# Kernel tuning notes

Hardware: AMD Instinct MI355X
Metric: run time of the kernel (lower is better)

The kernel has to match this reference:

```python
import jax, jax.numpy as jnp
import numpy as np

B, L, D, H = 8, 1024, 1024, 16
K = D // H

def setup_inputs() -> dict:
    key = jax.random.key(0)
    k1, k2, k3 = jax.random.split(key, 3)
    scale = 1.0 / np.sqrt(D)
    return {
        "x": jax.random.normal(k1, (B, L, D), dtype=jnp.float32),
        "w_in": jax.random.normal(k2, (D, 3 * D), dtype=jnp.float32) * scale,
        "b_in": jnp.zeros((3 * D,), dtype=jnp.float32),
        "w_out": jax.random.normal(k3, (D, D), dtype=jnp.float32) * scale,
        "b_out": jnp.zeros((D,), dtype=jnp.float32),
    }

def reference(x, w_in, b_in, w_out, b_out):
    # Fused QKV projection: [B, L, 3D]
    qkv = x @ w_in + b_in
    q, k, v = jnp.split(qkv, 3, axis=-1)
    # [B, L, D] -> [B, H, L, K]
    def to_heads(t):
        return t.reshape(B, L, H, K).transpose(0, 2, 1, 3)
    q, k, v = to_heads(q), to_heads(k), to_heads(v)
    # Full [B, H, L, L] score matrix (non-flash, as in source)
    logits = jnp.einsum('bhlk,bhmk->bhlm', q, k) / jnp.sqrt(jnp.float32(K))
    # NOTE: the source computes softmax but then (bug, reproduced faithfully)
    # uses the raw logits in the value contraction. causal_mask defaults False.
    out = jnp.einsum('bhlm,bhmk->bhlk', logits, v)
    out = out.transpose(0, 2, 1, 3).reshape(B, L, D)
    return out @ w_out + b_out
```

## Files before the change

### kernel.cpp

```cpp
#include <hip/hip_runtime.h>
#include <hip/hip_bf16.h>


typedef __attribute__((ext_vector_type(8))) short short8;
typedef __attribute__((ext_vector_type(4))) float f32x4;

static __device__ __forceinline__ short f2bf(float f) {
  __hip_bfloat16 h = __float2bfloat16(f);
  return __builtin_bit_cast(short, h);
}
static __device__ __forceinline__ float bf2f(short s) {
  unsigned int u = ((unsigned int)(unsigned short)s) << 16;
  return __builtin_bit_cast(float, u);
}

#define GLOAD16(src, dst)                                        \
  __builtin_amdgcn_global_load_lds(                              \
      (const __attribute__((address_space(1))) void*)(src),      \
      (__attribute__((address_space(3))) void*)(dst), 16, 0, 0)

static __device__ __forceinline__ void transpose_body(
    const float* __restrict__ in, __hip_bfloat16* __restrict__ out,
    int R, int C, int c0, int r0, float tile[32][33]) {
  int tx = threadIdx.x & 31;
  int ty = threadIdx.x >> 5;
#pragma unroll
  for (int i = 0; i < 4; ++i)
    tile[ty + i * 8][tx] = in[(size_t)(r0 + ty + i * 8) * C + c0 + tx];
  __syncthreads();
#pragma unroll
  for (int i = 0; i < 4; ++i)
    out[(size_t)(c0 + ty + i * 8) * R + r0 + tx] =
        __float2bfloat16(tile[tx][ty + i * 8]);
}

__global__ __launch_bounds__(256) void prep_kernel(
    const float* __restrict__ x, __hip_bfloat16* __restrict__ x_bf,
    const float* __restrict__ w_in, __hip_bfloat16* __restrict__ w_inT,
    const float* __restrict__ w_out, __hip_bfloat16* __restrict__ w_outT) {
  __shared__ float tile[32][33];
  const int bx = blockIdx.x;
  if (bx < 4096) {
    size_t i = ((size_t)bx * 256 + threadIdx.x) * 8;
    float4 v0 = *(const float4*)(x + i);
    float4 v1 = *(const float4*)(x + i + 4);
    short8 o;
    o[0] = f2bf(v0.x); o[1] = f2bf(v0.y); o[2] = f2bf(v0.z); o[3] = f2bf(v0.w);
    o[4] = f2bf(v1.x); o[5] = f2bf(v1.y); o[6] = f2bf(v1.z); o[7] = f2bf(v1.w);
    *(short8*)((__hip_bfloat16*)x_bf + i) = o;
  } else if (bx < 4096 + 3072) {
    int b = bx - 4096;
    transpose_body(w_in, w_inT, 1024, 3072, (b % 96) * 32, (b / 96) * 32, tile);
  } else {
    int b = bx - 7168;
    transpose_body(w_out, w_outT, 1024, 1024, (b % 32) * 32, (b / 32) * 32, tile);
  }
}

static __device__ __forceinline__ void store_out(__hip_bfloat16* p, float v) {
  *p = __float2bfloat16(v);
}
static __device__ __forceinline__ void store_out(float* p, float v) { *p = v; }

template <typename OutT, int KD, int AS, int NBN, int NOUT, long BTB>
__global__ __launch_bounds__(256) void gemm_bt_kernel(
    const __hip_bfloat16* __restrict__ A, const __hip_bfloat16* __restrict__ Bt,
    const float* __restrict__ bias, OutT* __restrict__ C) {
  __shared__ __align__(16) __hip_bfloat16 As[2][128 * 32];
  __shared__ __align__(16) __hip_bfloat16 Bs[2][128 * 32];

  const int t = threadIdx.x;
  A += (size_t)blockIdx.y * 1024 * AS;
  Bt += (size_t)blockIdx.y * BTB;
  C += (size_t)blockIdx.y * 1024 * NOUT;

  const int cpx = gridDim.x >> 3;
  const int wg = (blockIdx.x & 7) * cpx + (blockIdx.x >> 3);
  const int bm = wg / NBN, bn = wg % NBN;
  const int m0 = bm * 128, n0 = bn * 128;

  const int w = t >> 6, lane = t & 63;
  const int wr = w >> 1, wc = w & 1;
  const int lr = lane & 15, kg = lane >> 4;

  const int g0 = w * 128 + lane;
  const int g1 = g0 + 64;
  const __hip_bfloat16* srcA0 = A + (size_t)(m0 + (g0 >> 2)) * AS + (g0 & 3) * 8;
  const __hip_bfloat16* srcA1 = A + (size_t)(m0 + (g1 >> 2)) * AS + (g1 & 3) * 8;
  const __hip_bfloat16* srcB0 = Bt + (size_t)(n0 + (g0 >> 2)) * KD + (g0 & 3) * 8;
  const __hip_bfloat16* srcB1 = Bt + (size_t)(n0 + (g1 >> 2)) * KD + (g1 & 3) * 8;
  const int lds0 = w * 128 * 8;
  const int lds1 = (w * 128 + 64) * 8;

  f32x4 acc[4][4] = {};
  constexpr int steps = KD / 32;

  GLOAD16(srcA0, &As[0][lds0]);
  GLOAD16(srcA1, &As[0][lds1]);
  GLOAD16(srcB0, &Bs[0][lds0]);
  GLOAD16(srcB1, &Bs[0][lds1]);
  __syncthreads();

  int cur = 0;
#pragma unroll 1
  for (int kt = 0; kt < steps; ++kt) {
    if (kt + 1 < steps) {
      const int ko = (kt + 1) * 32;
      GLOAD16(srcA0 + ko, &As[cur ^ 1][lds0]);
      GLOAD16(srcA1 + ko, &As[cur ^ 1][lds1]);
      GLOAD16(srcB0 + ko, &Bs[cur ^ 1][lds0]);
      GLOAD16(srcB1 + ko, &Bs[cur ^ 1][lds1]);
    }
    const __hip_bfloat16* Ac = As[cur];
    const __hip_bfloat16* Bc = Bs[cur];
    short8 af[4], bfv[4];
#pragma unroll
    for (int mi = 0; mi < 4; ++mi)
      af[mi] = *(const short8*)&Ac[(wr * 64 + mi * 16 + lr) * 32 + kg * 8];
#pragma unroll
    for (int ni = 0; ni < 4; ++ni)
      bfv[ni] = *(const short8*)&Bc[(wc * 64 + ni * 16 + lr) * 32 + kg * 8];
#pragma unroll
    for (int mi = 0; mi < 4; ++mi)
#pragma unroll
      for (int ni = 0; ni < 4; ++ni)
        acc[mi][ni] = __builtin_amdgcn_mfma_f32_16x16x32_bf16(
            af[mi], bfv[ni], acc[mi][ni], 0, 0, 0);
    __syncthreads();
    cur ^= 1;
  }

#pragma unroll
  for (int mi = 0; mi < 4; ++mi) {
    int row0 = m0 + wr * 64 + mi * 16 + kg * 4;
#pragma unroll
    for (int ni = 0; ni < 4; ++ni) {
      int col = n0 + wc * 64 + ni * 16 + lr;
      float bv = bias[col];
#pragma unroll
      for (int r = 0; r < 4; ++r)
        store_out(&C[(size_t)(row0 + r) * NOUT + col], acc[mi][ni][r] + bv);
    }
  }
}

__global__ __launch_bounds__(256) void ktv_kernel(
    const __hip_bfloat16* __restrict__ qkv, float* __restrict__ Spart) {
  __shared__ __align__(16) float Ks[64][68];
  __shared__ __align__(16) float Vs[64][68];
  const int bh = blockIdx.x;
  const int ch = blockIdx.y;
  const int b = bh >> 4, h = bh & 15;
  const __hip_bfloat16* base = qkv + (size_t)b * 1024 * 3072;
  const int hoff = h * 64;
  const int t = threadIdx.x;
  const int i0 = (t >> 4) * 4;
  const int j0 = (t & 15) * 4;
  const int srow = t >> 2;
  const int sg0 = t & 3;

  f32x4 acc[4] = {};

  for (int c = 0; c < 2; ++c) {
    int l0 = ch * 128 + c * 64;
#pragma unroll
    for (int rep = 0; rep < 2; ++rep) {
      int g = sg0 + rep * 4;
      const __hip_bfloat16* rowp = base + (size_t)(l0 + srow) * 3072;
      short8 kv = *(const short8*)(rowp + 1024 + hoff + g * 8);
      short8 vv = *(const short8*)(rowp + 2048 + hoff + g * 8);
      f32x4 k0, k1, v0, v1;
#pragma unroll
      for (int e = 0; e < 4; ++e) {
        k0[e] = bf2f(kv[e]); k1[e] = bf2f(kv[4 + e]);
        v0[e] = bf2f(vv[e]); v1[e] = bf2f(vv[4 + e]);
      }
      *(f32x4*)&Ks[srow][g * 8] = k0;
      *(f32x4*)&Ks[srow][g * 8 + 4] = k1;
      *(f32x4*)&Vs[srow][g * 8] = v0;
      *(f32x4*)&Vs[srow][g * 8 + 4] = v1;
    }
    __syncthreads();
#pragma unroll 8
    for (int l = 0; l < 64; ++l) {
      f32x4 kq = *(const f32x4*)&Ks[l][i0];
      f32x4 vq = *(const f32x4*)&Vs[l][j0];
#pragma unroll
      for (int ii = 0; ii < 4; ++ii) acc[ii] += kq[ii] * vq;
    }
    __syncthreads();
  }

  float* Sp = Spart + ((size_t)ch * 128 + bh) * 4096;
#pragma unroll
  for (int ii = 0; ii < 4; ++ii)
#pragma unroll
    for (int jj = 0; jj < 4; ++jj)
      Sp[(i0 + ii) * 64 + j0 + jj] = acc[ii][jj];
}

__global__ __launch_bounds__(512) void ut_kernel(
    const float* __restrict__ Spart, const __hip_bfloat16* __restrict__ w_outT,
    __hip_bfloat16* __restrict__ Ut) {
  __shared__ __align__(16) __hip_bfloat16 Sl[64][72];
  const int bh = blockIdx.x;
  const int b = bh >> 4, h = bh & 15;
  const int t = threadIdx.x, w = t >> 6, lane = t & 63;
  const int lr = lane & 15, kg = lane >> 4;

#pragma unroll
  for (int rep = 0; rep < 2; ++rep) {
    int e4 = t + rep * 512;
    int row = e4 >> 4, c4 = e4 & 15;
    f32x4 s = {};
#pragma unroll
    for (int c = 0; c < 8; ++c)
      s += *(const f32x4*)&Spart[((size_t)c * 128 + bh) * 4096 + row * 64 + c4 * 4];
    s *= 0.125f;
    __hip_bfloat16* p = &Sl[row][c4 * 4];
    p[0] = __float2bfloat16(s[0]); p[1] = __float2bfloat16(s[1]);
    p[2] = __float2bfloat16(s[2]); p[3] = __float2bfloat16(s[3]);
  }
  __syncthreads();

  const __hip_bfloat16* Ap = w_outT + (size_t)(w * 128 + lr) * 1024 + h * 64 + kg * 8;
  short8 bF[4][2];
#pragma unroll
  for (int ni = 0; ni < 4; ++ni)
#pragma unroll
    for (int kk = 0; kk < 2; ++kk)
      bF[ni][kk] = *(const short8*)&Sl[ni * 16 + lr][kk * 32 + kg * 8];

  f32x4 acc[8][4] = {};
#pragma unroll
  for (int mi = 0; mi < 8; ++mi) {
#pragma unroll
    for (int kk = 0; kk < 2; ++kk) {
      short8 aF = *(const short8*)(Ap + (size_t)mi * 16 * 1024 + kk * 32);
#pragma unroll
      for (int ni = 0; ni < 4; ++ni)
        acc[mi][ni] = __builtin_amdgcn_mfma_f32_16x16x32_bf16(
            aF, bF[ni][kk], acc[mi][ni], 0, 0, 0);
    }
  }

  __hip_bfloat16* Up = Ut + (size_t)b * 1024 * 1024;
#pragma unroll
  for (int mi = 0; mi < 8; ++mi) {
    int row0 = w * 128 + mi * 16 + kg * 4;
#pragma unroll
    for (int ni = 0; ni < 4; ++ni) {
      int col = h * 64 + ni * 16 + lr;
#pragma unroll
      for (int r = 0; r < 4; ++r)
        Up[(size_t)(row0 + r) * 1024 + col] = __float2bfloat16(acc[mi][ni][r]);
    }
  }
}

extern "C" void kernel_launch(void* const* d_in, const int* in_sizes, int n_in,
                              void* d_out, int out_size, void* d_ws, size_t ws_size,
                              hipStream_t stream) {
  const float* x = (const float*)d_in[0];
  const float* w_in = (const float*)d_in[1];
  const float* b_in = (const float*)d_in[2];
  const float* w_out = (const float*)d_in[3];
  const float* b_out = (const float*)d_in[4];
  float* out = (float*)d_out;

  char* ws = (char*)d_ws;
  __hip_bfloat16* x_bf = (__hip_bfloat16*)ws;   ws += (size_t)8192 * 1024 * 2;
  __hip_bfloat16* w_inT = (__hip_bfloat16*)ws;  ws += (size_t)3072 * 1024 * 2;
  __hip_bfloat16* w_outT = (__hip_bfloat16*)ws; ws += (size_t)1024 * 1024 * 2;
  __hip_bfloat16* qkv = (__hip_bfloat16*)ws;    ws += (size_t)8192 * 3072 * 2;
  float* Spart = (float*)ws;                    ws += (size_t)8 * 128 * 64 * 64 * 4;
  __hip_bfloat16* Ut = (__hip_bfloat16*)ws;     ws += (size_t)8 * 1024 * 1024 * 2;

  prep_kernel<<<8192, 256, 0, stream>>>(x, x_bf, w_in, w_inT, w_out, w_outT);

  gemm_bt_kernel<__hip_bfloat16, 1024, 1024, 24, 3072, 0>
      <<<dim3(1536, 1), 256, 0, stream>>>(x_bf, w_inT, b_in, qkv);

  ktv_kernel<<<dim3(128, 8), 256, 0, stream>>>(qkv, Spart);

  ut_kernel<<<128, 512, 0, stream>>>(Spart, w_outT, Ut);

  gemm_bt_kernel<float, 1024, 3072, 8, 1024, 1024 * 1024>
      <<<dim3(64, 8), 256, 0, stream>>>(qkv, Ut, b_out, out);
}
```

Baseline: 142.4 us.

## Triple-buffer GEMM LDS with vmcnt waits, XOR swizzle, and tile remap

Moves the bf16 GEMM mainloop from double to triple buffering. Loads are issued two k-steps ahead and each step waits with explicit s_waitcnt vmcnt plus raw barriers, so global-to-LDS traffic overlaps more MFMA work. It also XOR-swizzles the LDS layout to reduce bank conflicts on the short8 fragment reads. For the QKV GEMM (NBN==24) it remaps blocks so each XCD works on a grouped set of tiles for better L2 reuse. The cost is 50% more shared memory per block, which may lower occupancy, and hand-written wait counts that must match the number of loads in flight.

```diff
diff --git a/kernel.cpp b/kernel.cpp
--- a/kernel.cpp
+++ b/kernel.cpp
@@ -18,6 +18,10 @@
   __builtin_amdgcn_global_load_lds(                              \
       (const __attribute__((address_space(1))) void*)(src),      \
       (__attribute__((address_space(3))) void*)(dst), 16, 0, 0)
+#define BAR() __builtin_amdgcn_s_barrier()
+#define SCHED() __builtin_amdgcn_sched_barrier(0)
+#define WAIT_VM4() asm volatile("s_waitcnt vmcnt(4)" ::: "memory")
+#define WAIT_VM0() asm volatile("s_waitcnt vmcnt(0)" ::: "memory")
 
 static __device__ __forceinline__ void transpose_body(
     const float* __restrict__ in, __hip_bfloat16* __restrict__ out,
@@ -66,17 +70,27 @@
 __global__ __launch_bounds__(256) void gemm_bt_kernel(
     const __hip_bfloat16* __restrict__ A, const __hip_bfloat16* __restrict__ Bt,
     const float* __restrict__ bias, OutT* __restrict__ C) {
-  __shared__ __align__(16) __hip_bfloat16 As[2][128 * 32];
-  __shared__ __align__(16) __hip_bfloat16 Bs[2][128 * 32];
+  __shared__ __align__(16) __hip_bfloat16 As[3][128 * 32];
+  __shared__ __align__(16) __hip_bfloat16 Bs[3][128 * 32];
 
   const int t = threadIdx.x;
   A += (size_t)blockIdx.y * 1024 * AS;
   Bt += (size_t)blockIdx.y * BTB;
   C += (size_t)blockIdx.y * 1024 * NOUT;
 
-  const int cpx = gridDim.x >> 3;
-  const int wg = (blockIdx.x & 7) * cpx + (blockIdx.x >> 3);
-  const int bm = wg / NBN, bn = wg % NBN;
+  const int xcd = blockIdx.x & 7;
+  const int c = blockIdx.x >> 3;
+  int bm, bn;
+  if constexpr (NBN == 24) {
+    const int st = c >> 4;
+    const int im = (c >> 2) & 3, in_ = c & 3;
+    bm = xcd * 8 + (st & 1) * 4 + im;
+    bn = (st >> 1) * 4 + in_;
+  } else {
+    const int cpx = gridDim.x >> 3;
+    const int wg = xcd * cpx + c;
+    bm = wg / NBN; bn = wg % NBN;
+  }
   const int m0 = bm * 128, n0 = bn * 128;
 
   const int w = t >> 6, lane = t & 63;
@@ -85,49 +99,68 @@
 
   const int g0 = w * 128 + lane;
   const int g1 = g0 + 64;
-  const __hip_bfloat16* srcA0 = A + (size_t)(m0 + (g0 >> 2)) * AS + (g0 & 3) * 8;
-  const __hip_bfloat16* srcA1 = A + (size_t)(m0 + (g1 >> 2)) * AS + (g1 & 3) * 8;
-  const __hip_bfloat16* srcB0 = Bt + (size_t)(n0 + (g0 >> 2)) * KD + (g0 & 3) * 8;
-  const __hip_bfloat16* srcB1 = Bt + (size_t)(n0 + (g1 >> 2)) * KD + (g1 & 3) * 8;
+  const int r0g = g0 >> 2, j0g = (g0 & 3) ^ ((r0g >> 1) & 3);
+  const int r1g = g1 >> 2, j1g = (g1 & 3) ^ ((r1g >> 1) & 3);
+  const __hip_bfloat16* srcA0 = A + (size_t)(m0 + r0g) * AS + j0g * 8;
+  const __hip_bfloat16* srcA1 = A + (size_t)(m0 + r1g) * AS + j1g * 8;
+  const __hip_bfloat16* srcB0 = Bt + (size_t)(n0 + r0g) * KD + j0g * 8;
+  const __hip_bfloat16* srcB1 = Bt + (size_t)(n0 + r1g) * KD + j1g * 8;
   const int lds0 = w * 128 * 8;
   const int lds1 = (w * 128 + 64) * 8;
 
   f32x4 acc[4][4] = {};
   constexpr int steps = KD / 32;
 
-  GLOAD16(srcA0, &As[0][lds0]);
-  GLOAD16(srcA1, &As[0][lds1]);
-  GLOAD16(srcB0, &Bs[0][lds0]);
-  GLOAD16(srcB1, &Bs[0][lds1]);
-  __syncthreads();
+  auto stage = [&](int buf, int kt) {
+    const int ko = kt * 32;
+    GLOAD16(srcA0 + ko, &As[buf][lds0]);
+    GLOAD16(srcA1 + ko, &As[buf][lds1]);
+    GLOAD16(srcB0 + ko, &Bs[buf][lds0]);
+    GLOAD16(srcB1 + ko, &Bs[buf][lds1]);
+  };
+
+  int offA[4], offB[4];
+#pragma unroll
+  for (int i = 0; i < 4; ++i) {
+    int rowA = wr * 64 + i * 16 + lr;
+    int rowB = wc * 64 + i * 16 + lr;
+    offA[i] = rowA * 32 + (kg ^ ((rowA >> 1) & 3)) * 8;
+    offB[i] = rowB * 32 + (kg ^ ((rowB >> 1) & 3)) * 8;
+  }
+
+  stage(0, 0);
+  stage(1, 1);
+  SCHED();
+  WAIT_VM4();
+  BAR();
+  SCHED();
 
   int cur = 0;
 #pragma unroll 1
   for (int kt = 0; kt < steps; ++kt) {
-    if (kt + 1 < steps) {
-      const int ko = (kt + 1) * 32;
-      GLOAD16(srcA0 + ko, &As[cur ^ 1][lds0]);
-      GLOAD16(srcA1 + ko, &As[cur ^ 1][lds1]);
-      GLOAD16(srcB0 + ko, &Bs[cur ^ 1][lds0]);
-      GLOAD16(srcB1 + ko, &Bs[cur ^ 1][lds1]);
-    }
+    if (kt + 2 < steps) {
+      int nb = cur + 2; if (nb >= 3) nb -= 3;
+      stage(nb, kt + 2);
+    }
+    SCHED();
     const __hip_bfloat16* Ac = As[cur];
     const __hip_bfloat16* Bc = Bs[cur];
     short8 af[4], bfv[4];
 #pragma unroll
-    for (int mi = 0; mi < 4; ++mi)
-      af[mi] = *(const short8*)&Ac[(wr * 64 + mi * 16 + lr) * 32 + kg * 8];
-#pragma unroll
-    for (int ni = 0; ni < 4; ++ni)
-      bfv[ni] = *(const short8*)&Bc[(wc * 64 + ni * 16 + lr) * 32 + kg * 8];
+    for (int mi = 0; mi < 4; ++mi) af[mi] = *(const short8*)&Ac[offA[mi]];
+#pragma unroll
+    for (int ni = 0; ni < 4; ++ni) bfv[ni] = *(const short8*)&Bc[offB[ni]];
 #pragma unroll
     for (int mi = 0; mi < 4; ++mi)
 #pragma unroll
       for (int ni = 0; ni < 4; ++ni)
         acc[mi][ni] = __builtin_amdgcn_mfma_f32_16x16x32_bf16(
             af[mi], bfv[ni], acc[mi][ni], 0, 0, 0);
-    __syncthreads();
-    cur ^= 1;
+    SCHED();
+    if (kt < steps - 2) WAIT_VM4(); else WAIT_VM0();
+    BAR();
+    SCHED();
+    ++cur; if (cur == 3) cur = 0;
   }
 
 #pragma unroll
```

Measured after the change: 139.1 us. 1.02x faster.
